# Performance work log

Hardware: AMD Instinct MI355X
Metric: run time of the kernel (lower is better)

The kernel has to match this reference:

```python
import jax, jax.numpy as jnp
import numpy as np

MAP_DS = 2.0
H, W = 512, 1024
MAXENT_WEIGHT = 1.0
EPS = 1e-5


def setup_inputs() -> dict:
    key = jax.random.key(0)
    k1, k2, k3 = jax.random.split(key, 3)
    B, T = 64, 256
    # Bounded random-walk trajectories in world coords (x in [0, H*ds), y in [0, W*ds))
    steps = jax.random.uniform(k1, (B, T, 2), minval=0.0, maxval=4.0)
    xy = jnp.cumsum(steps, axis=1) + 50.0
    xy = jnp.stack([jnp.clip(xy[..., 0], 0.0, H * MAP_DS - 1.0),
                    jnp.clip(xy[..., 1], 0.0, W * MAP_DS - 1.0)], axis=-1)
    # Pack into SE(2) pose matrices [B, T, 3, 3] with translation in [:2, 2]
    gt = jnp.tile(jnp.eye(3, dtype=jnp.float32), (B, T, 1, 1))
    gt = gt.at[:, :, 0, 2].set(xy[..., 0]).at[:, :, 1, 2].set(xy[..., 1])
    exp_svf = jax.random.uniform(k2, (B, H, W), dtype=jnp.float32)
    reward_preds = jax.random.normal(k3, (B, H, W), dtype=jnp.float32)
    return {"gt": gt, "exp_svf": exp_svf, "reward_preds": reward_preds}


def compute_expert_visitation(gt, max_steps):
    # gt: [B, T, 3, 3] SE(2) poses
    B = gt.shape[0]
    xy = gt[:, :, :2, 2] / MAP_DS                       # [B, T, 2] grid coords
    start = xy[:, :-1]                                  # [B, T-1, 2]
    end = xy[:, 1:]                                     # [B, T-1, 2]
    t = jnp.linspace(0.0, 1.0, max_steps, dtype=xy.dtype).reshape(1, 1, -1, 1)
    pts = start[:, :, None, :] + t * (end - start)[:, :, None, :]   # [B, T-1, S, 2]
    pts = pts.reshape(B, -1, 2)
    pts = jnp.concatenate([pts, xy[:, -1:]], axis=1)    # append last pose -> [B, N, 2]
    x = jnp.clip(pts[:, :, 0], 0, H - 1).astype(jnp.int32)
    y = jnp.clip(pts[:, :, 1], 0, W - 1).astype(jnp.int32)
    lin = x * W + y                                     # [B, N] flat indices
    flat = jnp.zeros((B, H * W), dtype=jnp.float32)
    flat = flat.at[jnp.arange(B)[:, None], lin].add(1.0)  # scatter-add histogram
    counts = jnp.minimum(flat, 1.0).reshape(B, H, W)      # binarize visitation
    return pts, counts


def reference(gt, exp_svf, reward_preds):
    # max_steps from concrete data, mirroring torch's .item() (eager, not traced)
    xy = np.asarray(gt)[:, :, :2, 2] / MAP_DS
    dist = np.linalg.norm(xy[:, 1:] - xy[:, :-1], axis=-1)
    max_steps = int(np.ceil(dist).max())
    interp_pts, svf = compute_expert_visitation(gt, max_steps)
    svf = svf / (svf.sum(axis=(1, 2), keepdims=True) + EPS)
    exp_svf = exp_svf / (exp_svf.sum(axis=(1, 2), keepdims=True) + EPS)
    svf_rewards = (svf * reward_preds).sum(axis=(1, 2))         # [B]
    exp_svf_rewards = (exp_svf * reward_preds).sum(axis=(1, 2))  # [B]
    visitation_loss = exp_svf_rewards.mean() - svf_rewards.mean()
    loss = MAXENT_WEIGHT * visitation_loss
    return loss, svf, interp_pts
```

## Files before the change

### kernel.cpp

```cpp
#include <hip/hip_runtime.h>

#define Bb 64
#define Tt 256
#define Hh 512
#define Ww 1024
#define HW (Hh * Ww)
#define EPSF 1e-5f

typedef float vf4 __attribute__((ext_vector_type(4)));


__global__ __launch_bounds__(256) void fused_reduce_zero(
        const float* __restrict__ exps, const float* __restrict__ rew,
        float* __restrict__ svf,
        double* __restrict__ esum_p, double* __restrict__ edot_p) {
    int b = blockIdx.x >> 6;
    int c = blockIdx.x & 63;
    size_t base = (size_t)b * HW + (size_t)c * 8192;

    const vf4* e4 = (const vf4*)(exps + base) + threadIdx.x;
    const vf4* r4 = (const vf4*)(rew + base) + threadIdx.x;

    vf4 ev[8], rv[8];
    #pragma unroll
    for (int k = 0; k < 8; ++k) ev[k] = e4[k * 256];
    #pragma unroll
    for (int k = 0; k < 8; ++k) rv[k] = r4[k * 256];

    {
        vf4* z4 = (vf4*)(svf + base + 3);
        vf4 z = {0.f, 0.f, 0.f, 0.f};
        #pragma unroll
        for (int k = 0; k < 8; ++k) {
            int i = threadIdx.x + k * 256;
            if (i < 2047) __builtin_nontemporal_store(z, &z4[i]);
        }
        if (threadIdx.x < 3) svf[base + threadIdx.x] = 0.0f;
        if (threadIdx.x == 3) svf[base + 8191] = 0.0f;
    }

    float es = 0.0f, ed = 0.0f;
    #pragma unroll
    for (int k = 0; k < 8; ++k) {
        vf4 e = ev[k], r = rv[k];
        es += (e.x + e.y) + (e.z + e.w);
        ed += (e.x * r.x + e.y * r.y) + (e.z * r.z + e.w * r.w);
    }

    for (int off = 32; off; off >>= 1) {
        es += __shfl_down(es, off);
        ed += __shfl_down(ed, off);
    }
    __shared__ float s_es[4], s_ed[4];
    int lane = threadIdx.x & 63, wv = threadIdx.x >> 6;
    if (lane == 0) { s_es[wv] = es; s_ed[wv] = ed; }
    __syncthreads();
    if (threadIdx.x == 0) {
        float tes = (s_es[0] + s_es[1]) + (s_es[2] + s_es[3]);
        float ted = (s_ed[0] + s_ed[1]) + (s_ed[2] + s_ed[3]);
        esum_p[blockIdx.x] = (double)tes;
        edot_p[blockIdx.x] = (double)ted;
    }
}

__device__ __forceinline__ void comp_pt(const float* __restrict__ gt, int b,
                                        int idx, int ms, int segN,
                                        float& px, float& py) {
    if (idx < segN) {
        int seg = idx / ms;
        int k = idx - seg * ms;
        const float* g0 = gt + (size_t)(b * Tt + seg) * 9;
        float sx = g0[2] * 0.5f, sy = g0[5] * 0.5f;
        float ex = g0[11] * 0.5f, ey = g0[14] * 0.5f;
        float t = (ms > 1) ? (float)k / (float)(ms - 1) : 0.0f;
        px = __fadd_rn(sx, __fmul_rn(t, __fsub_rn(ex, sx)));
        py = __fadd_rn(sy, __fmul_rn(t, __fsub_rn(ey, sy)));
    } else {
        const float* g0 = gt + (size_t)(b * Tt + (Tt - 1)) * 9;
        px = g0[2] * 0.5f;
        py = g0[5] * 0.5f;
    }
}

__device__ __forceinline__ int pt_cell(float px, float py) {
    int xi = (int)fminf(fmaxf(px, 0.0f), (float)(Hh - 1));
    int yi = (int)fminf(fmaxf(py, 0.0f), (float)(Ww - 1));
    return xi * Ww + yi;
}

__global__ __launch_bounds__(256) void scatter_batch(
        const float* __restrict__ gt, const float* __restrict__ rew,
        float* __restrict__ pts, float* __restrict__ svf,
        int* __restrict__ count_out, double* __restrict__ vdot_out,
        int ms, int P) {
    int b = blockIdx.x;
    int segN = (Tt - 1) * ms;

    int myCount = 0;
    float myV = 0.0f;
    for (int idx = threadIdx.x; idx < P; idx += 256) {
        float px, py;
        comp_pt(gt, b, idx, ms, segN, px, py);
        size_t pi = ((size_t)b * P + idx) * 2;
        pts[pi]     = px;
        pts[pi + 1] = py;
        int cell = pt_cell(px, py);
        bool claim;
        if (idx == 0) {
            claim = true;
        } else {
            float qx, qy;
            comp_pt(gt, b, idx - 1, ms, segN, qx, qy);
            claim = (pt_cell(qx, qy) != cell);
        }
        if (claim) {
            myCount++;
            myV += rew[(size_t)b * HW + cell];
        }
    }

    for (int off = 32; off; off >>= 1) {
        myCount += __shfl_down(myCount, off);
        myV     += __shfl_down(myV, off);
    }
    __shared__ int   sc[4];
    __shared__ float sv[4];
    __shared__ float s_recip;
    int lane = threadIdx.x & 63, wv = threadIdx.x >> 6;
    if (lane == 0) { sc[wv] = myCount; sv[wv] = myV; }
    __syncthreads();
    if (threadIdx.x == 0) {
        int tot  = (sc[0] + sc[1]) + (sc[2] + sc[3]);
        float tv = (sv[0] + sv[1]) + (sv[2] + sv[3]);
        count_out[b] = tot;
        vdot_out[b]  = (double)tv;
        s_recip = 1.0f / ((float)tot + EPSF);
    }
    __syncthreads();
    float recip = s_recip;

    for (int idx = threadIdx.x; idx < P; idx += 256) {
        size_t pi = ((size_t)b * P + idx) * 2;
        float px = pts[pi], py = pts[pi + 1];
        svf[(size_t)b * HW + pt_cell(px, py)] = recip;
    }
}

__global__ void loss_kernel(const double* __restrict__ esum_p,
                            const double* __restrict__ edot_p,
                            const double* __restrict__ vdot,
                            const int* __restrict__ count,
                            float* __restrict__ loss_out) {
    int b = threadIdx.x;
    double es = 0.0, ed = 0.0;
    #pragma unroll 8
    for (int c = 0; c < 64; ++c) {
        es += esum_p[b * 64 + c];
        ed += edot_p[b * 64 + c];
    }
    double e = ed / (es + 1e-5);
    double v = vdot[b] / ((double)count[b] + 1e-5);
    double term = e - v;
    for (int off = 32; off; off >>= 1) term += __shfl_down(term, off);
    if (b == 0) loss_out[0] = (float)(term / (double)Bb);
}

extern "C" void kernel_launch(void* const* d_in, const int* in_sizes, int n_in,
                              void* d_out, int out_size, void* d_ws, size_t ws_size,
                              hipStream_t stream) {
    const float* gt   = (const float*)d_in[0];
    const float* exps = (const float*)d_in[1];
    const float* rew  = (const float*)d_in[2];
    float* out = (float*)d_out;

    float* loss_out = out;
    float* svf = out + 1;
    int P  = (out_size - 1 - Bb * HW) / (Bb * 2);
    int ms = (P - 1) / (Tt - 1);
    float* pts = out + 1 + (size_t)Bb * HW;

    int*    count  = (int*)d_ws;
    double* vdot   = (double*)((char*)d_ws + 256);
    double* esum_p = (double*)((char*)d_ws + 768);
    double* edot_p = (double*)((char*)d_ws + 33536);

    fused_reduce_zero<<<Bb * 64, 256, 0, stream>>>(exps, rew, svf, esum_p, edot_p);
    scatter_batch<<<Bb, 256, 0, stream>>>(gt, rew, pts, svf, count, vdot, ms, P);
    loss_kernel<<<1, 64, 0, stream>>>(esum_p, edot_p, vdot, count, loss_out);
}
```

Before: 344.0 us.

## Merge reduction and scatter into one kernel, zero svf via memset

Zeroing of the svf output moves out of the reduction kernel into a hipMemsetAsync issued beforehand. The reduction and the per-batch scatter now run as one launch, with block ranges split by index, so scatter blocks can overlap the streaming reduction. Each reduction block now handles twice as much data, which halves the partial-sum count and shortens the final loss loop. The cost is an extra memset pass that writes the full 128MB svf buffer separately, plus longer work per block.

Measured after the change: 335.0 us. 1.03x faster.

```diff
diff --git a/kernel.cpp b/kernel.cpp
--- a/kernel.cpp
+++ b/kernel.cpp
@@ -7,61 +7,11 @@
 #define HW (Hh * Ww)
 #define EPSF 1e-5f
 
+#define RB 2048
+#define SB Bb
+
 typedef float vf4 __attribute__((ext_vector_type(4)));
 
-
-__global__ __launch_bounds__(256) void fused_reduce_zero(
-        const float* __restrict__ exps, const float* __restrict__ rew,
-        float* __restrict__ svf,
-        double* __restrict__ esum_p, double* __restrict__ edot_p) {
-    int b = blockIdx.x >> 6;
-    int c = blockIdx.x & 63;
-    size_t base = (size_t)b * HW + (size_t)c * 8192;
-
-    const vf4* e4 = (const vf4*)(exps + base) + threadIdx.x;
-    const vf4* r4 = (const vf4*)(rew + base) + threadIdx.x;
-
-    vf4 ev[8], rv[8];
-    #pragma unroll
-    for (int k = 0; k < 8; ++k) ev[k] = e4[k * 256];
-    #pragma unroll
-    for (int k = 0; k < 8; ++k) rv[k] = r4[k * 256];
-
-    {
-        vf4* z4 = (vf4*)(svf + base + 3);
-        vf4 z = {0.f, 0.f, 0.f, 0.f};
-        #pragma unroll
-        for (int k = 0; k < 8; ++k) {
-            int i = threadIdx.x + k * 256;
-            if (i < 2047) __builtin_nontemporal_store(z, &z4[i]);
-        }
-        if (threadIdx.x < 3) svf[base + threadIdx.x] = 0.0f;
-        if (threadIdx.x == 3) svf[base + 8191] = 0.0f;
-    }
-
-    float es = 0.0f, ed = 0.0f;
-    #pragma unroll
-    for (int k = 0; k < 8; ++k) {
-        vf4 e = ev[k], r = rv[k];
-        es += (e.x + e.y) + (e.z + e.w);
-        ed += (e.x * r.x + e.y * r.y) + (e.z * r.z + e.w * r.w);
-    }
-
-    for (int off = 32; off; off >>= 1) {
-        es += __shfl_down(es, off);
-        ed += __shfl_down(ed, off);
-    }
-    __shared__ float s_es[4], s_ed[4];
-    int lane = threadIdx.x & 63, wv = threadIdx.x >> 6;
-    if (lane == 0) { s_es[wv] = es; s_ed[wv] = ed; }
-    __syncthreads();
-    if (threadIdx.x == 0) {
-        float tes = (s_es[0] + s_es[1]) + (s_es[2] + s_es[3]);
-        float ted = (s_ed[0] + s_ed[1]) + (s_ed[2] + s_ed[3]);
-        esum_p[blockIdx.x] = (double)tes;
-        edot_p[blockIdx.x] = (double)ted;
-    }
-}
 
 __device__ __forceinline__ void comp_pt(const float* __restrict__ gt, int b,
                                         int idx, int ms, int segN,
@@ -88,61 +38,102 @@
     return xi * Ww + yi;
 }
 
-__global__ __launch_bounds__(256) void scatter_batch(
-        const float* __restrict__ gt, const float* __restrict__ rew,
+__global__ __launch_bounds__(256) void combined_kernel(
+        const float* __restrict__ exps, const float* __restrict__ rew,
+        const float* __restrict__ gt,
         float* __restrict__ pts, float* __restrict__ svf,
+        double* __restrict__ esum_p, double* __restrict__ edot_p,
         int* __restrict__ count_out, double* __restrict__ vdot_out,
         int ms, int P) {
-    int b = blockIdx.x;
-    int segN = (Tt - 1) * ms;
+    if (blockIdx.x < RB) {
+        int b = blockIdx.x >> 5;
+        int c = blockIdx.x & 31;
+        size_t base = (size_t)b * HW + (size_t)c * 16384;
 
-    int myCount = 0;
-    float myV = 0.0f;
-    for (int idx = threadIdx.x; idx < P; idx += 256) {
-        float px, py;
-        comp_pt(gt, b, idx, ms, segN, px, py);
-        size_t pi = ((size_t)b * P + idx) * 2;
-        pts[pi]     = px;
-        pts[pi + 1] = py;
-        int cell = pt_cell(px, py);
-        bool claim;
-        if (idx == 0) {
-            claim = true;
-        } else {
-            float qx, qy;
-            comp_pt(gt, b, idx - 1, ms, segN, qx, qy);
-            claim = (pt_cell(qx, qy) != cell);
+        float es = 0.0f, ed = 0.0f;
+        #pragma unroll
+        for (int j = 0; j < 2; ++j) {
+            const vf4* e4 = (const vf4*)(exps + base) + j * 2048 + threadIdx.x;
+            const vf4* r4 = (const vf4*)(rew  + base) + j * 2048 + threadIdx.x;
+            vf4 ev[8], rv[8];
+            #pragma unroll
+            for (int k = 0; k < 8; ++k) ev[k] = e4[k * 256];
+            #pragma unroll
+            for (int k = 0; k < 8; ++k) rv[k] = r4[k * 256];
+            #pragma unroll
+            for (int k = 0; k < 8; ++k) {
+                vf4 e = ev[k], r = rv[k];
+                es += (e.x + e.y) + (e.z + e.w);
+                ed += (e.x * r.x + e.y * r.y) + (e.z * r.z + e.w * r.w);
+            }
         }
-        if (claim) {
-            myCount++;
-            myV += rew[(size_t)b * HW + cell];
+
+        for (int off = 32; off; off >>= 1) {
+            es += __shfl_down(es, off);
+            ed += __shfl_down(ed, off);
         }
-    }
+        __shared__ float s_es[4], s_ed[4];
+        int lane = threadIdx.x & 63, wv = threadIdx.x >> 6;
+        if (lane == 0) { s_es[wv] = es; s_ed[wv] = ed; }
+        __syncthreads();
+        if (threadIdx.x == 0) {
+            float tes = (s_es[0] + s_es[1]) + (s_es[2] + s_es[3]);
+            float ted = (s_ed[0] + s_ed[1]) + (s_ed[2] + s_ed[3]);
+            esum_p[blockIdx.x] = (double)tes;
+            edot_p[blockIdx.x] = (double)ted;
+        }
+    } else {
+        int b = blockIdx.x - RB;
+        int segN = (Tt - 1) * ms;
 
-    for (int off = 32; off; off >>= 1) {
-        myCount += __shfl_down(myCount, off);
-        myV     += __shfl_down(myV, off);
-    }
-    __shared__ int   sc[4];
-    __shared__ float sv[4];
-    __shared__ float s_recip;
-    int lane = threadIdx.x & 63, wv = threadIdx.x >> 6;
-    if (lane == 0) { sc[wv] = myCount; sv[wv] = myV; }
-    __syncthreads();
-    if (threadIdx.x == 0) {
-        int tot  = (sc[0] + sc[1]) + (sc[2] + sc[3]);
-        float tv = (sv[0] + sv[1]) + (sv[2] + sv[3]);
-        count_out[b] = tot;
-        vdot_out[b]  = (double)tv;
-        s_recip = 1.0f / ((float)tot + EPSF);
-    }
-    __syncthreads();
-    float recip = s_recip;
+        int myCount = 0;
+        float myV = 0.0f;
+        for (int idx = threadIdx.x; idx < P; idx += 256) {
+            float px, py;
+            comp_pt(gt, b, idx, ms, segN, px, py);
+            size_t pi = ((size_t)b * P + idx) * 2;
+            pts[pi]     = px;
+            pts[pi + 1] = py;
+            int cell = pt_cell(px, py);
+            bool claim;
+            if (idx == 0) {
+                claim = true;
+            } else {
+                float qx, qy;
+                comp_pt(gt, b, idx - 1, ms, segN, qx, qy);
+                claim = (pt_cell(qx, qy) != cell);
+            }
+            if (claim) {
+                myCount++;
+                myV += rew[(size_t)b * HW + cell];
+            }
+        }
 
-    for (int idx = threadIdx.x; idx < P; idx += 256) {
-        size_t pi = ((size_t)b * P + idx) * 2;
-        float px = pts[pi], py = pts[pi + 1];
-        svf[(size_t)b * HW + pt_cell(px, py)] = recip;
+        for (int off = 32; off; off >>= 1) {
+            myCount += __shfl_down(myCount, off);
+            myV     += __shfl_down(myV, off);
+        }
+        __shared__ int   sc[4];
+        __shared__ float sv[4];
+        __shared__ float s_recip;
+        int lane = threadIdx.x & 63, wv = threadIdx.x >> 6;
+        if (lane == 0) { sc[wv] = myCount; sv[wv] = myV; }
+        __syncthreads();
+        if (threadIdx.x == 0) {
+            int tot  = (sc[0] + sc[1]) + (sc[2] + sc[3]);
+            float tv = (sv[0] + sv[1]) + (sv[2] + sv[3]);
+            count_out[b] = tot;
+            vdot_out[b]  = (double)tv;
+            s_recip = 1.0f / ((float)tot + EPSF);
+        }
+        __syncthreads();
+        float recip = s_recip;
+
+        for (int idx = threadIdx.x; idx < P; idx += 256) {
+            size_t pi = ((size_t)b * P + idx) * 2;
+            float px = pts[pi], py = pts[pi + 1];
+            svf[(size_t)b * HW + pt_cell(px, py)] = recip;
+        }
     }
 }
 
@@ -154,9 +145,9 @@
     int b = threadIdx.x;
     double es = 0.0, ed = 0.0;
     #pragma unroll 8
-    for (int c = 0; c < 64; ++c) {
-        es += esum_p[b * 64 + c];
-        ed += edot_p[b * 64 + c];
+    for (int c = 0; c < 32; ++c) {
+        es += esum_p[b * 32 + c];
+        ed += edot_p[b * 32 + c];
     }
     double e = ed / (es + 1e-5);
     double v = vdot[b] / ((double)count[b] + 1e-5);
@@ -182,9 +173,12 @@
     int*    count  = (int*)d_ws;
     double* vdot   = (double*)((char*)d_ws + 256);
     double* esum_p = (double*)((char*)d_ws + 768);
-    double* edot_p = (double*)((char*)d_ws + 33536);
+    double* edot_p = (double*)((char*)d_ws + 17152);
 
-    fused_reduce_zero<<<Bb * 64, 256, 0, stream>>>(exps, rew, svf, esum_p, edot_p);
-    scatter_batch<<<Bb, 256, 0, stream>>>(gt, rew, pts, svf, count, vdot, ms, P);
+    hipMemsetAsync(svf, 0, (size_t)Bb * HW * sizeof(float), stream);
+
+    combined_kernel<<<RB + SB, 256, 0, stream>>>(exps, rew, gt, pts, svf,
+                                                 esum_p, edot_p, count, vdot,
+                                                 ms, P);
     loss_kernel<<<1, 64, 0, stream>>>(esum_p, edot_p, vdot, count, loss_out);
 }
```
